# Performance work log

Measured on AMD Instinct MI355X. Metric: run time of the kernel, lower is better.

Reference implementation:

```python
import jax, jax.numpy as jnp
import numpy as np

B = 131072
DIM = 64
D_IN = 32
D_OUT = 32
HIDDEN = 512
N_BINS = 8
TAIL = 3.0


def setup_inputs() -> dict:
    key = jax.random.key(0)
    ks = jax.random.split(key, 7)
    x = jax.random.normal(ks[0], (B, DIM), dtype=jnp.float32)
    out_dim = D_OUT * (3 * N_BINS - 1)  # 32 * 23 = 736
    W1 = jax.random.normal(ks[1], (D_IN, HIDDEN), dtype=jnp.float32) / np.sqrt(D_IN)
    b1 = jnp.zeros((HIDDEN,), dtype=jnp.float32)
    W2 = jax.random.normal(ks[2], (HIDDEN, HIDDEN), dtype=jnp.float32) / np.sqrt(HIDDEN)
    b2 = jnp.zeros((HIDDEN,), dtype=jnp.float32)
    W3 = jax.random.normal(ks[3], (HIDDEN, out_dim), dtype=jnp.float32) / np.sqrt(HIDDEN)
    b3 = jnp.zeros((out_dim,), dtype=jnp.float32)
    return {"x": x, "W1": W1, "b1": b1, "W2": W2, "b2": b2, "W3": W3, "b3": b3}


def _gather(t, idx):
    # t: (..., K), idx: (...) -> (...,)
    return jnp.take_along_axis(t, idx[..., None], axis=-1)[..., 0]


def rq_spline_forward(x, widths, heights, derivatives, tail_bound=TAIL):
    K = widths.shape[-1]
    widths = jax.nn.softmax(widths, axis=-1) * 2 * tail_bound
    heights = jax.nn.softmax(heights, axis=-1) * 2 * tail_bound
    derivatives = jax.nn.softplus(derivatives)
    ones = jnp.ones_like(derivatives[..., :1])
    derivatives = jnp.concatenate([ones, derivatives, ones], axis=-1)  # (..., K+1)
    cumwidths = jnp.cumsum(widths, axis=-1)
    cumwidths = jnp.pad(cumwidths, [(0, 0)] * (cumwidths.ndim - 1) + [(1, 0)]) - tail_bound
    cumheights = jnp.cumsum(heights, axis=-1)
    cumheights = jnp.pad(cumheights, [(0, 0)] * (cumheights.ndim - 1) + [(1, 0)]) - tail_bound

    inside = (x >= -tail_bound) & (x <= tail_bound)
    xc = jnp.clip(x, -tail_bound + 1e-6, tail_bound - 1e-6)
    # searchsorted (left): number of knots strictly less than xc
    bin_idx = jnp.sum(cumwidths[..., 1:] < xc[..., None], axis=-1)
    bin_idx = jnp.clip(bin_idx, 0, K - 1)

    w_k = _gather(widths, bin_idx)
    h_k = _gather(heights, bin_idx)
    d_k = _gather(derivatives, bin_idx)
    d_k1 = _gather(derivatives[..., 1:], bin_idx)
    cw_k = _gather(cumwidths, bin_idx)
    ch_k = _gather(cumheights, bin_idx)

    xi = jnp.clip((xc - cw_k) / w_k, 1e-6, 1 - 1e-6)
    s_k = h_k / w_k
    num = h_k * (s_k * xi**2 + d_k * xi * (1 - xi))
    den = s_k + (d_k + d_k1 - 2 * s_k) * xi * (1 - xi)
    y_inside = ch_k + num / den
    log_det_inside = (
        jnp.log(s_k**2 * (d_k1 * xi**2 + 2 * s_k * xi * (1 - xi) + d_k * (1 - xi) ** 2) + 1e-8)
        - jnp.log(den**2 + 1e-8)
    )
    y = jnp.where(inside, y_inside, x)
    log_det = jnp.where(inside, log_det_inside, jnp.zeros_like(x))
    return y, log_det


def reference(x, W1, b1, W2, b2, W3, b3):
    # mask: first D_IN dims conditioned on, last D_OUT transformed
    x_masked = x[:, :D_IN]
    x_transform = x[:, D_IN:]
    h = jax.nn.relu(x_masked @ W1 + b1)
    h = jax.nn.relu(h @ W2 + b2)
    raw = h @ W3 + b3
    raw = raw.reshape(x.shape[0], D_OUT, 3 * N_BINS - 1)
    widths = raw[..., :N_BINS]
    heights = raw[..., N_BINS:2 * N_BINS]
    derivs = raw[..., 2 * N_BINS:]
    y_t, log_det = rq_spline_forward(x_transform, widths, heights, derivs, TAIL)
    y = jnp.concatenate([x_masked, y_t], axis=-1)
    return y, jnp.sum(log_det, axis=-1)
```

## Files before the change

kernel.cpp:

```cpp
#include <hip/hip_runtime.h>
#include <hip/hip_bf16.h>
#include <stdint.h>

typedef __bf16 bf16_t;
typedef _Float16 f16_t;
typedef _Float16 f16x8 __attribute__((ext_vector_type(8)));
typedef _Float16 f16x4 __attribute__((ext_vector_type(4)));
typedef float f32x4 __attribute__((ext_vector_type(4)));

#define HID 512
#define NRAW 736
#define NRAW_PAD 768
#define TAILB 3.0f

__device__ __forceinline__ void glds16(const void* g, void* s) {
  __builtin_amdgcn_global_load_lds(
      (const __attribute__((address_space(1))) void*)g,
      (__attribute__((address_space(3))) void*)s, 16, 0, 0);
}
__device__ __forceinline__ float frcp(float x) { return __builtin_amdgcn_rcpf(x); }

__global__ void detect_dtype(const void* x, int* flag) {
  __shared__ int s;
  if (threadIdx.x == 0) s = 0;
  __syncthreads();
  const bf16_t* xb = (const bf16_t*)x;
  int cnt = 0;
  for (int j = 0; j < 16; j++) {
    float v = (float)xb[threadIdx.x * 16 + j];
    if (!(v == v) || fabsf(v) > 64.0f) cnt++;
  }
  atomicAdd(&s, cnt);
  __syncthreads();
  if (threadIdx.x == 0) *flag = (s > 64) ? 1 : 0;
}

__global__ void conv_wb(const void* W1, const void* W2, const void* W3,
                        const void* b1, const void* b2, const void* b3,
                        f16_t* __restrict__ w1t, f16_t* __restrict__ w2t,
                        f16_t* __restrict__ w3t,
                        float* __restrict__ bf1, float* __restrict__ bf2,
                        float* __restrict__ bf3, const int* flagp) {
  const int flag = *flagp;
  auto rd = [&](const void* p, size_t idx) -> float {
    return flag ? ((const float*)p)[idx] : (float)((const bf16_t*)p)[idx];
  };
  int i = blockIdx.x * 256 + threadIdx.x;
  if (i < 512 * 32)  { w1t[i] = (f16_t)rd(W1, (size_t)(i & 31) * 512 + (i >> 5)); return; }
  i -= 512 * 32;
  if (i < 512 * 512) { w2t[i] = (f16_t)rd(W2, (size_t)(i & 511) * 512 + (i >> 9)); return; }
  i -= 512 * 512;
  if (i < NRAW_PAD * 512) {
    int n = i >> 9, k = i & 511;
    int ch = n / 24, e = n % 24;
    w3t[i] = (e < 23) ? (f16_t)rd(W3, (size_t)k * NRAW + ch * 23 + e) : (f16_t)0.0f;
    return;
  }
  i -= NRAW_PAD * 512;
  if (i < 512) { bf1[i] = rd(b1, i); return; }
  i -= 512;
  if (i < 512) { bf2[i] = rd(b2, i); return; }
  i -= 512;
  if (i < NRAW_PAD) {
    int ch = i / 24, e = i % 24;
    bf3[i] = (e < 23) ? rd(b3, (size_t)ch * 23 + e) : 0.0f;
  }
}

__global__ void convert_x(const void* x, void* __restrict__ outv,
                          const int* flagp, int n) {
  const int flag = *flagp;
  const int i0 = (blockIdx.x * 256 + threadIdx.x) * 8;
  if (i0 >= n) return;
  const int row = i0 >> 5, col = i0 & 31;
  const size_t src = (size_t)row * 64 + col;
  if (flag) {
    const float4* s4 = (const float4*)((const float*)x + src);
    float4* d4 = (float4*)((float*)outv + src);
    d4[0] = s4[0]; d4[1] = s4[1];
  } else {
    *(uint4*)((bf16_t*)outv + src) = *(const uint4*)((const bf16_t*)x + src);
  }
}

__global__ void ld_finalize(const float* __restrict__ ldp, void* __restrict__ outv,
                            const int* __restrict__ flagp, int M) {
  const int i = blockIdx.x * 256 + threadIdx.x;
  if (i >= M) return;
  float s = 0.f;
  #pragma unroll
  for (int n = 0; n < 4; n++) s += ldp[(size_t)n * M + i];
  if (*flagp) ((float*)outv)[(size_t)M * 64 + i] = s;
  else        ((bf16_t*)outv)[(size_t)M * 64 + i] = (bf16_t)s;
}

__launch_bounds__(256)
__global__ void gemm12(const void* __restrict__ xorig, const f16_t* __restrict__ W1t,
                       const float* __restrict__ b1, const f16_t* __restrict__ W2t,
                       const float* __restrict__ b2, f16_t* __restrict__ H2,
                       int r0, const int* __restrict__ flagp) {
  constexpr int BK = 64;
  __shared__ __align__(16) f16_t As[128 * BK], Bs[128 * BK];
  const int t = threadIdx.x;
  const int id = blockIdx.x;
  const int xcd = id & 7, s = id >> 3;
  const int n0 = (s & 3) * 128;
  const int m0 = ((s >> 2) * 8 + xcd) * 128;
  const int lrow = t >> 3, lcb = t & 7;
  const int lane = t & 63, w = t >> 6;
  const int wr = (w >> 1) * 64, wc = (w & 1) * 64, wc2 = (w & 1) * 32;
  const int lm = lane & 15, quad = lane >> 4;
  const int flag = *flagp;

  const f16_t* gb[4];
  f16_t* ldb[4];
  #pragma unroll
  for (int r = 0; r < 4; r++) {
    const int row = r * 32 + lrow;
    const int gc = (lcb ^ (row & 7)) * 8;
    gb[r] = W2t + (size_t)(n0 + row) * 512 + gc;
    ldb[r] = &Bs[row * BK + lcb * 8];
  }
  const f16x8* ap[4][2];
  const f16x8* bp[4][2];
  #pragma unroll
  for (int i = 0; i < 4; i++) {
    const int ra = wr + i * 16 + lm, rb = wc + i * 16 + lm;
    #pragma unroll
    for (int ksi = 0; ksi < 2; ksi++) {
      const int qb = ksi * 4 + quad;
      ap[i][ksi] = (const f16x8*)&As[ra * BK + ((qb ^ (ra & 7)) << 3)];
      bp[i][ksi] = (const f16x8*)&Bs[rb * BK + ((qb ^ (rb & 7)) << 3)];
    }
  }
  f16x8 xfr[4];
  #pragma unroll
  for (int i = 0; i < 4; i++) {
    const size_t xrow = (size_t)(r0 + m0 + wr + i * 16 + lm);
    if (flag) {
      const float* px = (const float*)xorig + xrow * 64 + quad * 8;
      const float4 a = *(const float4*)px;
      const float4 b = *(const float4*)(px + 4);
      f16x8 v;
      v[0] = (f16_t)a.x; v[1] = (f16_t)a.y; v[2] = (f16_t)a.z; v[3] = (f16_t)a.w;
      v[4] = (f16_t)b.x; v[5] = (f16_t)b.y; v[6] = (f16_t)b.z; v[7] = (f16_t)b.w;
      xfr[i] = v;
    } else {
      const bf16_t* px = (const bf16_t*)xorig + xrow * 64 + quad * 8;
      f16x8 v;
      #pragma unroll
      for (int j = 0; j < 8; j++) v[j] = (f16_t)(float)px[j];
      xfr[i] = v;
    }
  }
  const f16_t* w1p0 = W1t + (size_t)(wc2 + lm) * 32 + quad * 8;
  const f16_t* w1p1 = W1t + (size_t)(wc2 + 16 + lm) * 32 + quad * 8;
  const float* b1p0 = b1 + wc2 + 4 * quad;
  const float* b1p1 = b1 + wc2 + 16 + 4 * quad;
  f16_t* wadr[4][2];
  #pragma unroll
  for (int i = 0; i < 4; i++) {
    const int row = wr + i * 16 + lm;
    #pragma unroll
    for (int Tl = 0; Tl < 2; Tl++) {
      const int cb = (wc2 >> 3) + 2 * Tl + (quad >> 1);
      wadr[i][Tl] = &As[row * BK + ((cb ^ (row & 7)) << 3) + 4 * (quad & 1)];
    }
  }

  f32x4 acc[4][4] = {};
  f16x8 w1f0 = *(const f16x8*)w1p0;
  f16x8 w1f1 = *(const f16x8*)w1p1;

  #pragma unroll
  for (int k0i = 0; k0i < 8; k0i++) {
    const int k0 = k0i * 64;
    #pragma unroll
    for (int r = 0; r < 4; r++) glds16(gb[r] + k0, ldb[r]);
    const float4 bv0 = *(const float4*)(b1p0 + k0);
    const float4 bv1 = *(const float4*)(b1p1 + k0);
    f32x4 h[4][2];
    #pragma unroll
    for (int i = 0; i < 4; i++) {
      f32x4 z = {};
      h[i][0] = __builtin_amdgcn_mfma_f32_16x16x32_f16(w1f0, xfr[i], z, 0, 0, 0);
      h[i][1] = __builtin_amdgcn_mfma_f32_16x16x32_f16(w1f1, xfr[i], z, 0, 0, 0);
    }
    if (k0i < 7) {
      w1f0 = *(const f16x8*)(w1p0 + (size_t)(k0 + 64) * 32);
      w1f1 = *(const f16x8*)(w1p1 + (size_t)(k0 + 64) * 32);
    }
    __syncthreads();
    #pragma unroll
    for (int i = 0; i < 4; i++) {
      f16x4 v0, v1;
      v0[0] = (f16_t)fmaxf(h[i][0][0] + bv0.x, 0.0f);
      v0[1] = (f16_t)fmaxf(h[i][0][1] + bv0.y, 0.0f);
      v0[2] = (f16_t)fmaxf(h[i][0][2] + bv0.z, 0.0f);
      v0[3] = (f16_t)fmaxf(h[i][0][3] + bv0.w, 0.0f);
      v1[0] = (f16_t)fmaxf(h[i][1][0] + bv1.x, 0.0f);
      v1[1] = (f16_t)fmaxf(h[i][1][1] + bv1.y, 0.0f);
      v1[2] = (f16_t)fmaxf(h[i][1][2] + bv1.z, 0.0f);
      v1[3] = (f16_t)fmaxf(h[i][1][3] + bv1.w, 0.0f);
      *(f16x4*)wadr[i][0] = v0;
      *(f16x4*)wadr[i][1] = v1;
    }
    __syncthreads();
    #pragma unroll
    for (int ksi = 0; ksi < 2; ksi++) {
      f16x8 af[4], bf[4];
      #pragma unroll
      for (int i = 0; i < 4; i++) af[i] = *ap[i][ksi];
      #pragma unroll
      for (int j = 0; j < 4; j++) bf[j] = *bp[j][ksi];
      #pragma unroll
      for (int i = 0; i < 4; i++)
        #pragma unroll
        for (int j = 0; j < 4; j++)
          acc[i][j] = __builtin_amdgcn_mfma_f32_16x16x32_f16(af[i], bf[j], acc[i][j], 0, 0, 0);
    }
    if (k0i < 7) __syncthreads();
  }
  #pragma unroll
  for (int i = 0; i < 4; i++)
    #pragma unroll
    for (int j = 0; j < 4; j++) {
      const int col = n0 + wc + j * 16 + lm;
      const float bv = b2[col];
      #pragma unroll
      for (int r = 0; r < 4; r++) {
        const int rowi = m0 + wr + i * 16 + quad * 4 + r;
        H2[(size_t)rowi * HID + col] = (f16_t)fmaxf(acc[i][j][r] + bv, 0.0f);
      }
    }
}

#define RSH 200
#define SP1 0.5413248546f

__launch_bounds__(512, 4)
__global__ void gemm3_spline(const f16_t* __restrict__ A, const f16_t* __restrict__ Bt,
                             const float* __restrict__ bias,
                             const void* __restrict__ xorig,
                             void* __restrict__ outv, float* __restrict__ ldp,
                             int M, int r0, const int* __restrict__ flagp) {
  __shared__ __align__(16) f16_t lds[2 * 8192 + 2 * 12288];
  f16_t* As = lds;
  f16_t* Bs = lds + 2 * 8192;
  f16_t* rawh = lds;

  const int t = threadIdx.x;
  const int id = blockIdx.x;
  const int xcd = id & 7, sloc = id >> 3;
  const int cpx = gridDim.x >> 3;
  const int wg = xcd * cpx + sloc;
  const int ntile = wg & 3;
  const int m0 = (wg >> 2) * 128;
  const int n0 = ntile * 192;
  const int lane = t & 63, w = t >> 6;
  const int lm = lane & 15, quad = lane >> 4;
  const int wrow = (w >> 2) * 64, wcol = (w & 3) * 48;
  const int lrow = t >> 3, lcb = t & 7;
  const int flag = *flagp;

  const int gc = (lcb ^ (lrow & 7)) * 8;
  const f16_t* gA = A + (size_t)(m0 + lrow) * 512 + gc;
  const f16_t* gB = Bt + (size_t)(n0 + lrow) * 512 + gc;
  f16_t* ldA = As + lrow * 64 + lcb * 8;
  f16_t* ldB = Bs + lrow * 64 + lcb * 8;

  int aoff[4], boff[3];
  #pragma unroll
  for (int i = 0; i < 4; i++) {
    const int ra = wrow + i * 16 + lm;
    aoff[i] = ra * 64 + ((quad ^ (ra & 7)) << 3);
  }
  #pragma unroll
  for (int j = 0; j < 3; j++) {
    const int rb = wcol + j * 16 + lm;
    boff[j] = rb * 64 + ((quad ^ (rb & 7)) << 3);
  }

  const int prow = t >> 3, pch = t & 7;
  float xt_pre[2];
  #pragma unroll
  for (int e = 0; e < 2; e++) {
    const size_t gi = (size_t)(r0 + m0 + e * 64 + prow) * 64 + 32 + ntile * 8 + pch;
    xt_pre[e] = flag ? ((const float*)xorig)[gi] : (float)((const bf16_t*)xorig)[gi];
  }
  float bv3[3];
  #pragma unroll
  for (int j = 0; j < 3; j++) bv3[j] = bias[n0 + wcol + j * 16 + lm];

  #pragma unroll
  for (int r = 0; r < 2; r++) glds16(gA + r * 32768, ldA + r * 4096);
  #pragma unroll
  for (int r = 0; r < 3; r++) glds16(gB + r * 32768, ldB + r * 4096);
  __syncthreads();

  f32x4 acc[4][3] = {};

  #pragma unroll
  for (int t8 = 0; t8 < 8; t8++) {
    const f16_t* Ab = As + (t8 & 1) * 8192;
    const f16_t* Bb = Bs + (t8 & 1) * 12288;
    if (t8 < 7) {
      const int nb = (t8 + 1) & 1;
      #pragma unroll
      for (int r = 0; r < 2; r++)
        glds16(gA + r * 32768 + (t8 + 1) * 64, ldA + nb * 8192 + r * 4096);
      #pragma unroll
      for (int r = 0; r < 3; r++)
        glds16(gB + r * 32768 + (t8 + 1) * 64, ldB + nb * 12288 + r * 4096);
    }
    #pragma unroll
    for (int ksi = 0; ksi < 2; ksi++) {
      f16x8 af[4], bf[3];
      #pragma unroll
      for (int i = 0; i < 4; i++)
        af[i] = *(const f16x8*)(Ab + (aoff[i] ^ (ksi << 5)));
      #pragma unroll
      for (int j = 0; j < 3; j++)
        bf[j] = *(const f16x8*)(Bb + (boff[j] ^ (ksi << 5)));
      __builtin_amdgcn_s_setprio(1);
      #pragma unroll
      for (int i = 0; i < 4; i++)
        #pragma unroll
        for (int j = 0; j < 3; j++)
          acc[i][j] = __builtin_amdgcn_mfma_f32_16x16x32_f16(af[i], bf[j], acc[i][j], 0, 0, 0);
      __builtin_amdgcn_s_setprio(0);
    }
    __syncthreads();
  }

  #pragma unroll
  for (int i = 0; i < 4; i++)
    #pragma unroll
    for (int j = 0; j < 3; j++) {
      const int col = wcol + j * 16 + lm;
      #pragma unroll
      for (int r = 0; r < 4; r++)
        rawh[(wrow + i * 16 + quad * 4 + r) * RSH + col] = (f16_t)(acc[i][j][r] + bv3[j]);
    }
  __syncthreads();

  #pragma unroll
  for (int e = 0; e < 2; e++) {
    const int row = e * 64 + prow;
    const f16_t* c16 = &rawh[row * RSH + pch * 24];
    const f16x8 v0 = *(const f16x8*)(c16);
    const f16x8 v1 = *(const f16x8*)(c16 + 8);
    const f16x8 v2 = *(const f16x8*)(c16 + 16);
    float wa[8], ha[8], da[7];
    #pragma unroll
    for (int j = 0; j < 8; j++) { wa[j] = (float)v0[j]; ha[j] = (float)v1[j]; }
    #pragma unroll
    for (int j = 0; j < 7; j++) da[j] = (float)v2[j];

    const float xt = xt_pre[e];
    const bool inside = (xt >= -TAILB) && (xt <= TAILB);
    const float xc = fminf(fmaxf(xt, -TAILB + 1e-6f), TAILB - 1e-6f);

    float mw = wa[0], mh = ha[0];
    #pragma unroll
    for (int j = 1; j < 8; j++) { mw = fmaxf(mw, wa[j]); mh = fmaxf(mh, ha[j]); }
    float ew[8], eh[8], sew = 0.f, seh = 0.f;
    #pragma unroll
    for (int j = 0; j < 8; j++) {
      ew[j] = __expf(wa[j] - mw); sew += ew[j];
      eh[j] = __expf(ha[j] - mh); seh += eh[j];
    }
    const float wsc = 6.0f * frcp(sew), hsc = 6.0f * frcp(seh);
    #pragma unroll
    for (int j = 0; j < 8; j++) { ew[j] *= wsc; eh[j] *= hsc; }

    float accw = -TAILB, runh = -TAILB;
    float cwk = -TAILB, chk = -TAILB;
    float wk = ew[0], hk = eh[0];
    float dkr = SP1, dk1r = da[0];
    #pragma unroll
    for (int i = 0; i < 7; i++) {
      accw += ew[i];
      runh += eh[i];
      const bool cond = accw < xc;
      cwk  = cond ? accw : cwk;
      chk  = cond ? runh : chk;
      wk   = cond ? ew[i + 1] : wk;
      hk   = cond ? eh[i + 1] : hk;
      dkr  = cond ? da[i] : dkr;
      dk1r = cond ? ((i == 6) ? SP1 : da[i + 1]) : dk1r;
    }
    const float dk  = fmaxf(dkr, 0.0f)  + __logf(1.0f + __expf(-fabsf(dkr)));
    const float dk1 = fmaxf(dk1r, 0.0f) + __logf(1.0f + __expf(-fabsf(dk1r)));

    const float rwk = frcp(wk);
    float xi = (xc - cwk) * rwk;
    xi = fminf(fmaxf(xi, 1e-6f), 1.0f - 1e-6f);
    const float om = 1.0f - xi;
    const float sl = hk * rwk;
    const float num = hk * (sl * xi * xi + dk * xi * om);
    const float den = sl + (dk + dk1 - 2.0f * sl) * xi * om;
    const float y_in = chk + num * frcp(den);
    const float t1 = sl * sl * (dk1 * xi * xi + 2.0f * sl * xi * om + dk * om * om);
    const float ld_in = __logf(t1 + 1e-8f) - __logf(den * den + 1e-8f);

    const float yv = inside ? y_in : xt;
    const float ldv = inside ? ld_in : 0.0f;

    const size_t grow = (size_t)(r0 + m0 + row);
    if (flag) ((float*)outv)[grow * 64 + 32 + ntile * 8 + pch] = yv;
    else      ((bf16_t*)outv)[grow * 64 + 32 + ntile * 8 + pch] = (bf16_t)yv;

    float l = ldv + __shfl_down(ldv, 1, 8);
    l += __shfl_down(l, 2, 8);
    l += __shfl_down(l, 4, 8);
    if ((t & 7) == 0) ldp[(size_t)ntile * M + grow] = l;
  }
}

extern "C" void kernel_launch(void* const* d_in, const int* in_sizes, int n_in,
                              void* d_out, int out_size, void* d_ws, size_t ws_size,
                              hipStream_t stream) {
  const void* x  = d_in[0];
  const void* W1 = d_in[1];
  const void* b1 = d_in[2];
  const void* W2 = d_in[3];
  const void* b2 = d_in[4];
  const void* W3 = d_in[5];
  const void* b3 = d_in[6];
  const int M = in_sizes[0] / 64;

  char* ws = (char*)d_ws;
  size_t off = 0;
  auto alloc = [&](size_t bytes) {
    void* p = ws + off;
    off += (bytes + 255) & ~(size_t)255;
    return p;
  };
  int*   flag = (int*)alloc(256);
  float* bf1  = (float*)alloc(512 * 4);
  float* bf2  = (float*)alloc(512 * 4);
  float* bf3  = (float*)alloc(NRAW_PAD * 4);
  f16_t* W1t  = (f16_t*)alloc((size_t)512 * 32 * 2);
  f16_t* W2t  = (f16_t*)alloc((size_t)512 * 512 * 2);
  f16_t* W3t  = (f16_t*)alloc((size_t)NRAW_PAD * 512 * 2);
  float* ldp  = (float*)alloc((size_t)8 * M * 4);

  const size_t per_row = (size_t)HID * 2;
  size_t avail = (ws_size > off + 4096) ? (ws_size - off - 4096) : 0;
  long rows = (long)(avail / per_row);
  rows -= rows % 1024;
  if (rows > M) rows = M;
  if (rows < 1024) rows = 1024;

  f16_t* h2 = (f16_t*)alloc((size_t)rows * HID * 2);

  detect_dtype<<<1, 256, 0, stream>>>(x, flag);
  conv_wb<<<2631, 256, 0, stream>>>(W1, W2, W3, b1, b2, b3,
                                    W1t, W2t, W3t, bf1, bf2, bf3, flag);
  convert_x<<<(M * 32 / 8 + 255) / 256, 256, 0, stream>>>(x, d_out, flag, M * 32);

  for (int r0 = 0; r0 < M; r0 += (int)rows) {
    const int mc = (int)((M - r0 < rows) ? (M - r0) : rows);
    const int mt128 = mc / 128;
    gemm12<<<mt128 * 4, 256, 0, stream>>>(x, W1t, bf1, W2t, bf2, h2, r0, flag);
    gemm3_spline<<<mt128 * 4, 512, 0, stream>>>(
        h2, W3t, bf3, x, d_out, ldp, M, r0, flag);
  }
  ld_finalize<<<(M + 255) / 256, 256, 0, stream>>>(ldp, d_out, flag, M);
}
```

Measured before the change: 327.0 us.

## Double-buffer LDS tiles in fused gemm12 to overlap next-tile fill with MFMA

```diff
diff --git a/kernel.cpp b/kernel.cpp
--- a/kernel.cpp
+++ b/kernel.cpp
@@ -100,7 +100,8 @@
                        const float* __restrict__ b2, f16_t* __restrict__ H2,
                        int r0, const int* __restrict__ flagp) {
   constexpr int BK = 64;
-  __shared__ __align__(16) f16_t As[128 * BK], Bs[128 * BK];
+  constexpr int BUF = 128 * BK;
+  __shared__ __align__(16) f16_t As[2 * BUF], Bs[2 * BUF];
   const int t = threadIdx.x;
   const int id = blockIdx.x;
   const int xcd = id & 7, s = id >> 3;
@@ -121,16 +122,15 @@
     gb[r] = W2t + (size_t)(n0 + row) * 512 + gc;
     ldb[r] = &Bs[row * BK + lcb * 8];
   }
-  const f16x8* ap[4][2];
-  const f16x8* bp[4][2];
+  int apo[4][2], bpo[4][2];
   #pragma unroll
   for (int i = 0; i < 4; i++) {
     const int ra = wr + i * 16 + lm, rb = wc + i * 16 + lm;
     #pragma unroll
     for (int ksi = 0; ksi < 2; ksi++) {
       const int qb = ksi * 4 + quad;
-      ap[i][ksi] = (const f16x8*)&As[ra * BK + ((qb ^ (ra & 7)) << 3)];
-      bp[i][ksi] = (const f16x8*)&Bs[rb * BK + ((qb ^ (rb & 7)) << 3)];
+      apo[i][ksi] = ra * BK + ((qb ^ (ra & 7)) << 3);
+      bpo[i][ksi] = rb * BK + ((qb ^ (rb & 7)) << 3);
     }
   }
   f16x8 xfr[4];
@@ -157,69 +157,97 @@
   const f16_t* w1p1 = W1t + (size_t)(wc2 + 16 + lm) * 32 + quad * 8;
   const float* b1p0 = b1 + wc2 + 4 * quad;
   const float* b1p1 = b1 + wc2 + 16 + 4 * quad;
-  f16_t* wadr[4][2];
+  int woff[4][2];
   #pragma unroll
   for (int i = 0; i < 4; i++) {
     const int row = wr + i * 16 + lm;
     #pragma unroll
     for (int Tl = 0; Tl < 2; Tl++) {
       const int cb = (wc2 >> 3) + 2 * Tl + (quad >> 1);
-      wadr[i][Tl] = &As[row * BK + ((cb ^ (row & 7)) << 3) + 4 * (quad & 1)];
+      woff[i][Tl] = row * BK + ((cb ^ (row & 7)) << 3) + 4 * (quad & 1);
     }
   }
 
   f32x4 acc[4][4] = {};
-  f16x8 w1f0 = *(const f16x8*)w1p0;
-  f16x8 w1f1 = *(const f16x8*)w1p1;
-
-  #pragma unroll
-  for (int k0i = 0; k0i < 8; k0i++) {
-    const int k0 = k0i * 64;
-    #pragma unroll
-    for (int r = 0; r < 4; r++) glds16(gb[r] + k0, ldb[r]);
-    const float4 bv0 = *(const float4*)(b1p0 + k0);
-    const float4 bv1 = *(const float4*)(b1p1 + k0);
-    f32x4 h[4][2];
+
+  {
+    f16x8 w1f0 = *(const f16x8*)w1p0;
+    f16x8 w1f1 = *(const f16x8*)w1p1;
+    const float4 bv0 = *(const float4*)b1p0;
+    const float4 bv1 = *(const float4*)b1p1;
+    #pragma unroll
+    for (int r = 0; r < 4; r++) glds16(gb[r], ldb[r]);
     #pragma unroll
     for (int i = 0; i < 4; i++) {
       f32x4 z = {};
-      h[i][0] = __builtin_amdgcn_mfma_f32_16x16x32_f16(w1f0, xfr[i], z, 0, 0, 0);
-      h[i][1] = __builtin_amdgcn_mfma_f32_16x16x32_f16(w1f1, xfr[i], z, 0, 0, 0);
-    }
-    if (k0i < 7) {
-      w1f0 = *(const f16x8*)(w1p0 + (size_t)(k0 + 64) * 32);
-      w1f1 = *(const f16x8*)(w1p1 + (size_t)(k0 + 64) * 32);
-    }
-    __syncthreads();
-    #pragma unroll
-    for (int i = 0; i < 4; i++) {
+      const f32x4 h0 = __builtin_amdgcn_mfma_f32_16x16x32_f16(w1f0, xfr[i], z, 0, 0, 0);
+      const f32x4 h1 = __builtin_amdgcn_mfma_f32_16x16x32_f16(w1f1, xfr[i], z, 0, 0, 0);
       f16x4 v0, v1;
-      v0[0] = (f16_t)fmaxf(h[i][0][0] + bv0.x, 0.0f);
-      v0[1] = (f16_t)fmaxf(h[i][0][1] + bv0.y, 0.0f);
-      v0[2] = (f16_t)fmaxf(h[i][0][2] + bv0.z, 0.0f);
-      v0[3] = (f16_t)fmaxf(h[i][0][3] + bv0.w, 0.0f);
-      v1[0] = (f16_t)fmaxf(h[i][1][0] + bv1.x, 0.0f);
-      v1[1] = (f16_t)fmaxf(h[i][1][1] + bv1.y, 0.0f);
-      v1[2] = (f16_t)fmaxf(h[i][1][2] + bv1.z, 0.0f);
-      v1[3] = (f16_t)fmaxf(h[i][1][3] + bv1.w, 0.0f);
-      *(f16x4*)wadr[i][0] = v0;
-      *(f16x4*)wadr[i][1] = v1;
-    }
-    __syncthreads();
+      v0[0] = (f16_t)fmaxf(h0[0] + bv0.x, 0.0f);
+      v0[1] = (f16_t)fmaxf(h0[1] + bv0.y, 0.0f);
+      v0[2] = (f16_t)fmaxf(h0[2] + bv0.z, 0.0f);
+      v0[3] = (f16_t)fmaxf(h0[3] + bv0.w, 0.0f);
+      v1[0] = (f16_t)fmaxf(h1[0] + bv1.x, 0.0f);
+      v1[1] = (f16_t)fmaxf(h1[1] + bv1.y, 0.0f);
+      v1[2] = (f16_t)fmaxf(h1[2] + bv1.z, 0.0f);
+      v1[3] = (f16_t)fmaxf(h1[3] + bv1.w, 0.0f);
+      *(f16x4*)&As[woff[i][0]] = v0;
+      *(f16x4*)&As[woff[i][1]] = v1;
+    }
+  }
+  f16x8 w1fa = *(const f16x8*)(w1p0 + (size_t)64 * 32);
+  f16x8 w1fb = *(const f16x8*)(w1p1 + (size_t)64 * 32);
+  float4 bva = *(const float4*)(b1p0 + 64);
+  float4 bvb = *(const float4*)(b1p1 + 64);
+  __syncthreads();
+
+  #pragma unroll
+  for (int k = 0; k < 8; k++) {
+    const int cur = k & 1, nb = cur ^ 1;
+    if (k < 7) {
+      #pragma unroll
+      for (int r = 0; r < 4; r++)
+        glds16(gb[r] + (k + 1) * 64, ldb[r] + nb * BUF);
+      #pragma unroll
+      for (int i = 0; i < 4; i++) {
+        f32x4 z = {};
+        const f32x4 h0 = __builtin_amdgcn_mfma_f32_16x16x32_f16(w1fa, xfr[i], z, 0, 0, 0);
+        const f32x4 h1 = __builtin_amdgcn_mfma_f32_16x16x32_f16(w1fb, xfr[i], z, 0, 0, 0);
+        f16x4 v0, v1;
+        v0[0] = (f16_t)fmaxf(h0[0] + bva.x, 0.0f);
+        v0[1] = (f16_t)fmaxf(h0[1] + bva.y, 0.0f);
+        v0[2] = (f16_t)fmaxf(h0[2] + bva.z, 0.0f);
+        v0[3] = (f16_t)fmaxf(h0[3] + bva.w, 0.0f);
+        v1[0] = (f16_t)fmaxf(h1[0] + bvb.x, 0.0f);
+        v1[1] = (f16_t)fmaxf(h1[1] + bvb.y, 0.0f);
+        v1[2] = (f16_t)fmaxf(h1[2] + bvb.z, 0.0f);
+        v1[3] = (f16_t)fmaxf(h1[3] + bvb.w, 0.0f);
+        *(f16x4*)&As[nb * BUF + woff[i][0]] = v0;
+        *(f16x4*)&As[nb * BUF + woff[i][1]] = v1;
+      }
+      if (k < 6) {
+        w1fa = *(const f16x8*)(w1p0 + (size_t)(k + 2) * 64 * 32);
+        w1fb = *(const f16x8*)(w1p1 + (size_t)(k + 2) * 64 * 32);
+        bva = *(const float4*)(b1p0 + (k + 2) * 64);
+        bvb = *(const float4*)(b1p1 + (k + 2) * 64);
+      }
+    }
     #pragma unroll
     for (int ksi = 0; ksi < 2; ksi++) {
       f16x8 af[4], bf[4];
       #pragma unroll
-      for (int i = 0; i < 4; i++) af[i] = *ap[i][ksi];
-      #pragma unroll
-      for (int j = 0; j < 4; j++) bf[j] = *bp[j][ksi];
+      for (int i = 0; i < 4; i++) af[i] = *(const f16x8*)&As[cur * BUF + apo[i][ksi]];
+      #pragma unroll
+      for (int j = 0; j < 4; j++) bf[j] = *(const f16x8*)&Bs[cur * BUF + bpo[j][ksi]];
+      __builtin_amdgcn_s_setprio(1);
       #pragma unroll
       for (int i = 0; i < 4; i++)
         #pragma unroll
         for (int j = 0; j < 4; j++)
           acc[i][j] = __builtin_amdgcn_mfma_f32_16x16x32_f16(af[i], bf[j], acc[i][j], 0, 0, 0);
-    }
-    if (k0i < 7) __syncthreads();
+      __builtin_amdgcn_s_setprio(0);
+    }
+    if (k < 7) __syncthreads();
   }
   #pragma unroll
   for (int i = 0; i < 4; i++)
```

Result: no change. 333.5 us (+2.0%).
